# Optimization experiments

Measured on AMD Instinct MI355X. Metric: run time of the kernel, lower is better.

Reference implementation:

```python
import jax, jax.numpy as jnp
import numpy as np

B, S, H = 32, 2048, 1024


def setup_inputs() -> dict:
    key = jax.random.key(0)
    ks = jax.random.split(key, 8)
    scale = 1.0 / np.sqrt(H)
    return {
        "query": jax.random.normal(ks[0], (B, 1, H), dtype=jnp.float32),
        "keys": jax.random.normal(ks[1], (B, S, H), dtype=jnp.float32),
        "Wa_w": jax.random.uniform(ks[2], (H, H), jnp.float32, -scale, scale),
        "Wa_b": jax.random.uniform(ks[3], (H,), jnp.float32, -scale, scale),
        "Ua_w": jax.random.uniform(ks[4], (H, H), jnp.float32, -scale, scale),
        "Ua_b": jax.random.uniform(ks[5], (H,), jnp.float32, -scale, scale),
        "Va_w": jax.random.uniform(ks[6], (1, H), jnp.float32, -scale, scale),
        "Va_b": jax.random.uniform(ks[7], (1,), jnp.float32, -scale, scale),
        "idx": 0,
    }


def reference(query, keys, Wa_w, Wa_b, Ua_w, Ua_b, Va_w, Va_b, idx):
    # torch Linear: y = x @ W.T + b
    q_proj = jnp.einsum("bqh,oh->bqo", query, Wa_w) + Wa_b   # (B,1,H)
    k_proj = jnp.einsum("bsh,oh->bso", keys, Ua_w) + Ua_b    # (B,S,H)
    energy = jnp.tanh(q_proj + k_proj)                        # (B,S,H) broadcast over S
    scores = jnp.einsum("bsh,h->bs", energy, Va_w[0]) + Va_b[0]  # (B,S)
    weights = jax.nn.softmax(scores, axis=-1)[:, None, :]     # (B,1,S)
    context = jnp.einsum("bqs,bsh->bqh", weights, keys)       # (B,1,H)
    return (context, weights)
```

## Files before the change

kernel.cpp:

```cpp
#include <hip/hip_runtime.h>
#include <hip/hip_bf16.h>
#include <math.h>


#define B_ 32
#define S_ 2048
#define H_ 1024
#define M_ (B_ * S_)

#define CONV_BLOCKS 8192
#define UA_BLOCKS 32
#define QP_BLOCKS 512

typedef __bf16 bf16x8 __attribute__((ext_vector_type(8)));
typedef float floatx4 __attribute__((ext_vector_type(4)));

__device__ inline unsigned bf16_rne(float f) {
  unsigned u = __builtin_bit_cast(unsigned, f);
  return (u + 0x7fffu + ((u >> 16) & 1u)) >> 16;
}
__device__ inline unsigned pk2(float x, float y) {
  return bf16_rne(x) | (bf16_rne(y) << 16);
}

__device__ inline float fast_tanh(float x) {
  const float xc = fminf(fmaxf(x, -8.f), 8.f);
  const float e = __expf(2.f * xc);
  return (e - 1.f) * __builtin_amdgcn_rcpf(e + 1.f);
}

#define GLDS(g, l)                                                    \
  __builtin_amdgcn_global_load_lds(                                   \
      (const __attribute__((address_space(1))) void*)(g),             \
      (__attribute__((address_space(3))) void*)(l), 16, 0, 0)

__device__ inline uint4 conv8(const float4* s2) {
  const float4 a = s2[0], b = s2[1];
  uint4 o;
  o.x = pk2(a.x, a.y); o.y = pk2(a.z, a.w);
  o.z = pk2(b.x, b.y); o.w = pk2(b.z, b.w);
  return o;
}

__global__ __launch_bounds__(256) void prep_kernel(
    const float* __restrict__ keys, const float* __restrict__ Ua_w,
    const float* __restrict__ query, const float* __restrict__ Wa_w,
    const float* __restrict__ Wa_b, const float* __restrict__ Ua_b,
    unsigned short* __restrict__ kbf, unsigned short* __restrict__ ubf,
    float* __restrict__ qp, int do_convert) {
  const int blk = blockIdx.x;
  const int tid = threadIdx.x;
  if (blk < CONV_BLOCKS) {
    if (!do_convert) return;
    const int tg = blk * 256 + tid;
#pragma unroll
    for (int c = 0; c < 4; ++c) {
      const size_t idx = (size_t)c * 2097152 + tg;
      ((uint4*)kbf)[idx] = conv8((const float4*)keys + idx * 2);
    }
  } else if (blk < CONV_BLOCKS + UA_BLOCKS) {
    if (!do_convert) return;
    const int tg = (blk - CONV_BLOCKS) * 256 + tid;
#pragma unroll
    for (int c = 0; c < 16; ++c) {
      const size_t idx = (size_t)c * 8192 + tg;
      ((uint4*)ubf)[idx] = conv8((const float4*)Ua_w + idx * 2);
    }
  } else {
    const int bl = blk - CONV_BLOCKS - UA_BLOCKS;
    const int b = bl >> 4;
    const int os = (bl & 15) * 64;
    const int lane = tid & 63;
    const int w = tid >> 6;
    __shared__ float qsh[H_];
    *(float4*)&qsh[tid * 4] = *(const float4*)(query + (size_t)b * H_ + tid * 4);
    __syncthreads();
    for (int t = 0; t < 16; ++t) {
      const int o = os + w * 16 + t;
      const float* wr = Wa_w + (size_t)o * H_;
      float p = 0.f;
#pragma unroll
      for (int j = 0; j < 16; ++j) p += wr[lane + 64 * j] * qsh[lane + 64 * j];
#pragma unroll
      for (int m = 32; m; m >>= 1) p += __shfl_xor(p, m);
      if (lane == 0) qp[b * H_ + o] = p + Wa_b[o] + Ua_b[o];
    }
  }
}

__device__ inline void swizzle_rc(int idx, int& rb, int& cb) {
  cb = (idx >> 3) & 7;
  rb = (idx & 7) | ((idx >> 6) << 3);
}
__device__ inline int chunk_f(int r) { return (r & 3) ^ ((r >> 2) & 3); }

__global__ __launch_bounds__(256) void scores_bf16_kernel(
    const unsigned short* __restrict__ kbf, const unsigned short* __restrict__ ubf,
    const float* __restrict__ qp, const float* __restrict__ Va_w,
    float* __restrict__ sp) {
  const int tid = threadIdx.x;
  int rb, cb;
  swizzle_rc(blockIdx.x, rb, cb);
  const int row0 = rb * 128, c0 = cb * 128;
  const int bq = row0 >> 11;
  const int lane = tid & 63;
  const int w = tid >> 6;
  const int wm = w >> 1, wn = w & 1;
  const int q4 = lane >> 4, n16 = lane & 15;

  __shared__ __align__(16) unsigned short Asm[128][32];
  __shared__ __align__(16) unsigned short Bsm[128][32];
  __shared__ float red[2][128];

  floatx4 acc[4][4];
#pragma unroll
  for (int i = 0; i < 4; ++i)
#pragma unroll
    for (int j = 0; j < 4; ++j) acc[i][j] = {0.f, 0.f, 0.f, 0.f};

  const int r0a = w * 32;
  const int lr = lane >> 2;
  const int lc = ((lane & 3) ^ chunk_f(lr)) * 8;
  const unsigned short* gA0 = kbf + (size_t)(row0 + r0a + lr) * H_ + lc;
  const unsigned short* gA1 = kbf + (size_t)(row0 + r0a + 16 + lr) * H_ + lc;
  const unsigned short* gB0 = ubf + (size_t)(c0 + r0a + lr) * H_ + lc;
  const unsigned short* gB1 = ubf + (size_t)(c0 + r0a + 16 + lr) * H_ + lc;
  unsigned short* lA0 = &Asm[r0a][0];
  unsigned short* lA1 = &Asm[r0a + 16][0];
  unsigned short* lB0 = &Bsm[r0a][0];
  unsigned short* lB1 = &Bsm[r0a + 16][0];

  const int fn = chunk_f(n16);

  for (int kt = 0; kt < 32; ++kt) {
    const int k0 = kt * 32;
    __syncthreads();
    GLDS(gA0 + k0, lA0);
    GLDS(gA1 + k0, lA1);
    GLDS(gB0 + k0, lB0);
    GLDS(gB1 + k0, lB1);
    __syncthreads();
    bf16x8 af[4], bfr[4];
#pragma unroll
    for (int i = 0; i < 4; ++i)
      af[i] = *(const bf16x8*)&Asm[wm * 64 + i * 16 + n16][(q4 ^ fn) * 8];
#pragma unroll
    for (int j = 0; j < 4; ++j)
      bfr[j] = *(const bf16x8*)&Bsm[wn * 64 + j * 16 + n16][(q4 ^ fn) * 8];
#pragma unroll
    for (int i = 0; i < 4; ++i)
#pragma unroll
      for (int j = 0; j < 4; ++j)
        acc[i][j] = __builtin_amdgcn_mfma_f32_16x16x32_bf16(af[i], bfr[j], acc[i][j], 0, 0, 0);
  }

  float rsum[4][4];
#pragma unroll
  for (int i = 0; i < 4; ++i)
#pragma unroll
    for (int r = 0; r < 4; ++r) rsum[i][r] = 0.f;
#pragma unroll
  for (int j = 0; j < 4; ++j) {
    const int col = c0 + wn * 64 + j * 16 + n16;
    const float qv = qp[bq * H_ + col];
    const float vv = Va_w[col];
#pragma unroll
    for (int i = 0; i < 4; ++i)
#pragma unroll
      for (int r = 0; r < 4; ++r)
        rsum[i][r] += fast_tanh(acc[i][j][r] + qv) * vv;
  }
#pragma unroll
  for (int i = 0; i < 4; ++i)
#pragma unroll
    for (int r = 0; r < 4; ++r) {
      float v = rsum[i][r];
      v += __shfl_xor(v, 1);
      v += __shfl_xor(v, 2);
      v += __shfl_xor(v, 4);
      v += __shfl_xor(v, 8);
      rsum[i][r] = v;
    }
  if (n16 == 0) {
#pragma unroll
    for (int i = 0; i < 4; ++i)
#pragma unroll
      for (int r = 0; r < 4; ++r)
        red[wn][wm * 64 + i * 16 + q4 * 4 + r] = rsum[i][r];
  }
  __syncthreads();
  if (tid < 128) sp[(size_t)cb * M_ + row0 + tid] = red[0][tid] + red[1][tid];
}

__global__ __launch_bounds__(256) void scores_f32_kernel(
    const float* __restrict__ keys, const float* __restrict__ Ua_w,
    const float* __restrict__ qp, const float* __restrict__ Va_w,
    float* __restrict__ sp) {
  const int tid = threadIdx.x;
  int rb, cb;
  swizzle_rc(blockIdx.x, rb, cb);
  const int row0 = rb * 128, c0 = cb * 128;
  const int bq = row0 >> 11;
  const int lane = tid & 63;
  const int w = tid >> 6;
  const int wm = w >> 1, wn = w & 1;
  const int q4 = lane >> 4, n16 = lane & 15;

  __shared__ __align__(16) unsigned short Asm[128][40];
  __shared__ __align__(16) unsigned short Bsm[128][40];
  __shared__ float red[2][128];

  floatx4 acc[4][4];
#pragma unroll
  for (int i = 0; i < 4; ++i)
#pragma unroll
    for (int j = 0; j < 4; ++j) acc[i][j] = {0.f, 0.f, 0.f, 0.f};

  for (int kt = 0; kt < 32; ++kt) {
    const int k0 = kt * 32;
    __syncthreads();
#pragma unroll
    for (int rep = 0; rep < 4; ++rep) {
      const int idx4 = rep * 256 + tid;
      const int r = idx4 >> 3;
      const int c4 = (idx4 & 7) << 2;
      const float4 va = *(const float4*)(keys + (size_t)(row0 + r) * H_ + k0 + c4);
      *(uint2*)&Asm[r][c4] = make_uint2(pk2(va.x, va.y), pk2(va.z, va.w));
      const float4 vb = *(const float4*)(Ua_w + (size_t)(c0 + r) * H_ + k0 + c4);
      *(uint2*)&Bsm[r][c4] = make_uint2(pk2(vb.x, vb.y), pk2(vb.z, vb.w));
    }
    __syncthreads();
    bf16x8 af[4], bfr[4];
#pragma unroll
    for (int i = 0; i < 4; ++i)
      af[i] = *(const bf16x8*)&Asm[wm * 64 + i * 16 + n16][q4 * 8];
#pragma unroll
    for (int j = 0; j < 4; ++j)
      bfr[j] = *(const bf16x8*)&Bsm[wn * 64 + j * 16 + n16][q4 * 8];
#pragma unroll
    for (int i = 0; i < 4; ++i)
#pragma unroll
      for (int j = 0; j < 4; ++j)
        acc[i][j] = __builtin_amdgcn_mfma_f32_16x16x32_bf16(af[i], bfr[j], acc[i][j], 0, 0, 0);
  }

  float rsum[4][4];
#pragma unroll
  for (int i = 0; i < 4; ++i)
#pragma unroll
    for (int r = 0; r < 4; ++r) rsum[i][r] = 0.f;
#pragma unroll
  for (int j = 0; j < 4; ++j) {
    const int col = c0 + wn * 64 + j * 16 + n16;
    const float qv = qp[bq * H_ + col];
    const float vv = Va_w[col];
#pragma unroll
    for (int i = 0; i < 4; ++i)
#pragma unroll
      for (int r = 0; r < 4; ++r)
        rsum[i][r] += fast_tanh(acc[i][j][r] + qv) * vv;
  }
#pragma unroll
  for (int i = 0; i < 4; ++i)
#pragma unroll
    for (int r = 0; r < 4; ++r) {
      float v = rsum[i][r];
      v += __shfl_xor(v, 1);
      v += __shfl_xor(v, 2);
      v += __shfl_xor(v, 4);
      v += __shfl_xor(v, 8);
      rsum[i][r] = v;
    }
  if (n16 == 0) {
#pragma unroll
    for (int i = 0; i < 4; ++i)
#pragma unroll
      for (int r = 0; r < 4; ++r)
        red[wn][wm * 64 + i * 16 + q4 * 4 + r] = rsum[i][r];
  }
  __syncthreads();
  if (tid < 128) sp[(size_t)cb * M_ + row0 + tid] = red[0][tid] + red[1][tid];
}

__global__ __launch_bounds__(256) void softmax_kernel(
    const float* __restrict__ sp, float* __restrict__ sw) {
  const int b = blockIdx.x, tid = threadIdx.x;
  float v[8];
#pragma unroll
  for (int k = 0; k < 8; ++k) {
    const size_t base = (size_t)b * S_ + tid + 256 * k;
    float s = 0.f;
#pragma unroll
    for (int j = 0; j < 8; ++j) s += sp[(size_t)j * M_ + base];
    v[k] = s;
  }
  float mx = v[0];
#pragma unroll
  for (int k = 1; k < 8; ++k) mx = fmaxf(mx, v[k]);
#pragma unroll
  for (int m = 32; m; m >>= 1) mx = fmaxf(mx, __shfl_xor(mx, m));
  __shared__ float sred[4], ssum[4];
  if ((tid & 63) == 0) sred[tid >> 6] = mx;
  __syncthreads();
  mx = fmaxf(fmaxf(sred[0], sred[1]), fmaxf(sred[2], sred[3]));
  float e[8], s = 0.f;
#pragma unroll
  for (int k = 0; k < 8; ++k) { e[k] = __expf(v[k] - mx); s += e[k]; }
#pragma unroll
  for (int m = 32; m; m >>= 1) s += __shfl_xor(s, m);
  if ((tid & 63) == 0) ssum[tid >> 6] = s;
  __syncthreads();
  s = ssum[0] + ssum[1] + ssum[2] + ssum[3];
  const float inv = 1.0f / s;
#pragma unroll
  for (int k = 0; k < 8; ++k) sw[b * S_ + tid + 256 * k] = e[k] * inv;
}

__global__ __launch_bounds__(256) void context1_kernel(
    const float* __restrict__ keys, const float* __restrict__ weights,
    float* __restrict__ pctx) {
  const int b = blockIdx.x >> 6;
  const int ch = blockIdx.x & 63;
  const int s0 = ch * 32;
  const int h4 = threadIdx.x;
  const float4* kp4 = (const float4*)(keys + (size_t)(b * S_ + s0) * H_) + h4;
  const float4* wp4 = (const float4*)(weights + b * S_ + s0);
  float4 acc = {0.f, 0.f, 0.f, 0.f};
#pragma unroll
  for (int sq = 0; sq < 8; ++sq) {
    const float4 wv = wp4[sq];
    const float4 k0 = kp4[(sq * 4 + 0) * 256];
    const float4 k1 = kp4[(sq * 4 + 1) * 256];
    const float4 k2 = kp4[(sq * 4 + 2) * 256];
    const float4 k3 = kp4[(sq * 4 + 3) * 256];
    acc.x += wv.x * k0.x + wv.y * k1.x + wv.z * k2.x + wv.w * k3.x;
    acc.y += wv.x * k0.y + wv.y * k1.y + wv.z * k2.y + wv.w * k3.y;
    acc.z += wv.x * k0.z + wv.y * k1.z + wv.z * k2.z + wv.w * k3.z;
    acc.w += wv.x * k0.w + wv.y * k1.w + wv.z * k2.w + wv.w * k3.w;
  }
  *(float4*)(pctx + ((size_t)(b * 64 + ch)) * H_ + h4 * 4) = acc;
}

__global__ __launch_bounds__(256) void context2_kernel(
    const float* __restrict__ pctx, float* __restrict__ ctx) {
  const int b = blockIdx.x;
  const int h4 = threadIdx.x * 4;
  float4 acc = {0.f, 0.f, 0.f, 0.f};
#pragma unroll 8
  for (int c = 0; c < 64; ++c) {
    const float4 v = *(const float4*)(pctx + ((size_t)(b * 64 + c)) * H_ + h4);
    acc.x += v.x; acc.y += v.y; acc.z += v.z; acc.w += v.w;
  }
  *(float4*)(ctx + b * H_ + h4) = acc;
}

extern "C" void kernel_launch(void* const* d_in, const int* in_sizes, int n_in,
                              void* d_out, int out_size, void* d_ws, size_t ws_size,
                              hipStream_t stream) {
  const float* query = (const float*)d_in[0];
  const float* keys  = (const float*)d_in[1];
  const float* Wa_w  = (const float*)d_in[2];
  const float* Wa_b  = (const float*)d_in[3];
  const float* Ua_w  = (const float*)d_in[4];
  const float* Ua_b  = (const float*)d_in[5];
  const float* Va_w  = (const float*)d_in[6];

  float* out = (float*)d_out;
  float* ctx = out;
  float* sw  = out + B_ * H_;

  const size_t qpb = (size_t)B_ * H_ * 4;
  const size_t spb = (size_t)8 * M_ * 4;
  const size_t pcb = (size_t)B_ * 64 * H_ * 4;
  const size_t kb  = (size_t)M_ * H_ * 2;
  const size_t ub  = (size_t)H_ * H_ * 2;
  float* qp = (float*)d_ws;
  float* sp = (float*)((char*)d_ws + qpb);
  float* pctx = (float*)((char*)d_ws + qpb + spb);
  unsigned short* kbf = (unsigned short*)((char*)d_ws + qpb + spb + pcb);
  unsigned short* ubf = (unsigned short*)((char*)d_ws + qpb + spb + pcb + kb);
  const bool fast = ws_size >= qpb + spb + pcb + kb + ub;

  prep_kernel<<<CONV_BLOCKS + UA_BLOCKS + QP_BLOCKS, 256, 0, stream>>>(
      keys, Ua_w, query, Wa_w, Wa_b, Ua_b, kbf, ubf, qp, fast ? 1 : 0);
  if (fast) {
    scores_bf16_kernel<<<4096, 256, 0, stream>>>(kbf, ubf, qp, Va_w, sp);
  } else {
    scores_f32_kernel<<<4096, 256, 0, stream>>>(keys, Ua_w, qp, Va_w, sp);
  }
  softmax_kernel<<<B_, 256, 0, stream>>>(sp, sw);
  context1_kernel<<<2048, 256, 0, stream>>>(keys, sw, pctx);
  context2_kernel<<<B_, 256, 0, stream>>>(pctx, ctx);
}
```

Measured before the change: 632.4 us.

## Fuse fp32-to-bf16 key conversion into the scores GEMM A-tile load

Removes the separate pass that converted the full keys tensor to bf16 in a workspace buffer. The scores kernel now reads fp32 keys directly, converts them in registers with packed bf16 conversion instructions, and stores them to LDS, prefetching the next K-slice into registers during the current step. This saves writing and re-reading a 128MB intermediate. In exchange, each 128-column block re-reads fp32 keys (twice the bytes per tile) and loses the async global-to-LDS path for A.

```diff
diff --git a/kernel.cpp b/kernel.cpp
--- a/kernel.cpp
+++ b/kernel.cpp
@@ -8,9 +8,8 @@
 #define H_ 1024
 #define M_ (B_ * S_)
 
-#define CONV_BLOCKS 8192
+#define QP_BLOCKS 512
 #define UA_BLOCKS 32
-#define QP_BLOCKS 512
 
 typedef __bf16 bf16x8 __attribute__((ext_vector_type(8)));
 typedef float floatx4 __attribute__((ext_vector_type(4)));
@@ -21,6 +20,11 @@
 }
 __device__ inline unsigned pk2(float x, float y) {
   return bf16_rne(x) | (bf16_rne(y) << 16);
+}
+__device__ inline unsigned cvtpk(float x, float y) {
+  unsigned r;
+  asm("v_cvt_pk_bf16_f32 %0, %1, %2" : "=v"(r) : "v"(x), "v"(y));
+  return r;
 }
 
 __device__ inline float fast_tanh(float x) {
@@ -43,33 +47,15 @@
 }
 
 __global__ __launch_bounds__(256) void prep_kernel(
-    const float* __restrict__ keys, const float* __restrict__ Ua_w,
-    const float* __restrict__ query, const float* __restrict__ Wa_w,
-    const float* __restrict__ Wa_b, const float* __restrict__ Ua_b,
-    unsigned short* __restrict__ kbf, unsigned short* __restrict__ ubf,
-    float* __restrict__ qp, int do_convert) {
+    const float* __restrict__ Ua_w, const float* __restrict__ query,
+    const float* __restrict__ Wa_w, const float* __restrict__ Wa_b,
+    const float* __restrict__ Ua_b, unsigned short* __restrict__ ubf,
+    float* __restrict__ qp, int do_ua) {
   const int blk = blockIdx.x;
   const int tid = threadIdx.x;
-  if (blk < CONV_BLOCKS) {
-    if (!do_convert) return;
-    const int tg = blk * 256 + tid;
-#pragma unroll
-    for (int c = 0; c < 4; ++c) {
-      const size_t idx = (size_t)c * 2097152 + tg;
-      ((uint4*)kbf)[idx] = conv8((const float4*)keys + idx * 2);
-    }
-  } else if (blk < CONV_BLOCKS + UA_BLOCKS) {
-    if (!do_convert) return;
-    const int tg = (blk - CONV_BLOCKS) * 256 + tid;
-#pragma unroll
-    for (int c = 0; c < 16; ++c) {
-      const size_t idx = (size_t)c * 8192 + tg;
-      ((uint4*)ubf)[idx] = conv8((const float4*)Ua_w + idx * 2);
-    }
-  } else {
-    const int bl = blk - CONV_BLOCKS - UA_BLOCKS;
-    const int b = bl >> 4;
-    const int os = (bl & 15) * 64;
+  if (blk < QP_BLOCKS) {
+    const int b = blk >> 4;
+    const int os = (blk & 15) * 64;
     const int lane = tid & 63;
     const int w = tid >> 6;
     __shared__ float qsh[H_];
@@ -85,6 +71,14 @@
       for (int m = 32; m; m >>= 1) p += __shfl_xor(p, m);
       if (lane == 0) qp[b * H_ + o] = p + Wa_b[o] + Ua_b[o];
     }
+  } else {
+    if (!do_ua) return;
+    const int tg = (blk - QP_BLOCKS) * 256 + tid;
+#pragma unroll
+    for (int c = 0; c < 16; ++c) {
+      const size_t idx = (size_t)c * 8192 + tg;
+      ((uint4*)ubf)[idx] = conv8((const float4*)Ua_w + idx * 2);
+    }
   }
 }
 
@@ -94,8 +88,8 @@
 }
 __device__ inline int chunk_f(int r) { return (r & 3) ^ ((r >> 2) & 3); }
 
-__global__ __launch_bounds__(256) void scores_bf16_kernel(
-    const unsigned short* __restrict__ kbf, const unsigned short* __restrict__ ubf,
+__global__ __launch_bounds__(256) void scores_af32_kernel(
+    const float* __restrict__ keys, const unsigned short* __restrict__ ubf,
     const float* __restrict__ qp, const float* __restrict__ Va_w,
     float* __restrict__ sp) {
   const int tid = threadIdx.x;
@@ -121,24 +115,41 @@
   const int r0a = w * 32;
   const int lr = lane >> 2;
   const int lc = ((lane & 3) ^ chunk_f(lr)) * 8;
-  const unsigned short* gA0 = kbf + (size_t)(row0 + r0a + lr) * H_ + lc;
-  const unsigned short* gA1 = kbf + (size_t)(row0 + r0a + 16 + lr) * H_ + lc;
   const unsigned short* gB0 = ubf + (size_t)(c0 + r0a + lr) * H_ + lc;
   const unsigned short* gB1 = ubf + (size_t)(c0 + r0a + 16 + lr) * H_ + lc;
-  unsigned short* lA0 = &Asm[r0a][0];
-  unsigned short* lA1 = &Asm[r0a + 16][0];
   unsigned short* lB0 = &Bsm[r0a][0];
   unsigned short* lB1 = &Bsm[r0a + 16][0];
 
+  const int ar = tid >> 1;
+  const int ac0 = (tid & 1) * 2;
+  const float* gA = keys + (size_t)(row0 + ar) * H_ + ac0 * 8;
+  unsigned short* lA0 = &Asm[ar][((ac0 ^ chunk_f(ar)) & 3) * 8];
+  unsigned short* lA1 = &Asm[ar][(((ac0 + 1) ^ chunk_f(ar)) & 3) * 8];
+
   const int fn = chunk_f(n16);
+
+  float4 a0 = *(const float4*)(gA + 0);
+  float4 a1 = *(const float4*)(gA + 4);
+  float4 a2 = *(const float4*)(gA + 8);
+  float4 a3 = *(const float4*)(gA + 12);
 
   for (int kt = 0; kt < 32; ++kt) {
     const int k0 = kt * 32;
     __syncthreads();
-    GLDS(gA0 + k0, lA0);
-    GLDS(gA1 + k0, lA1);
     GLDS(gB0 + k0, lB0);
     GLDS(gB1 + k0, lB1);
+    uint4 u0, u1;
+    u0.x = cvtpk(a0.x, a0.y); u0.y = cvtpk(a0.z, a0.w);
+    u0.z = cvtpk(a1.x, a1.y); u0.w = cvtpk(a1.z, a1.w);
+    u1.x = cvtpk(a2.x, a2.y); u1.y = cvtpk(a2.z, a2.w);
+    u1.z = cvtpk(a3.x, a3.y); u1.w = cvtpk(a3.z, a3.w);
+    *(uint4*)lA0 = u0;
+    *(uint4*)lA1 = u1;
+    const int kn = ((kt + 1) & 31) * 32;
+    a0 = *(const float4*)(gA + kn + 0);
+    a1 = *(const float4*)(gA + kn + 4);
+    a2 = *(const float4*)(gA + kn + 8);
+    a3 = *(const float4*)(gA + kn + 12);
     __syncthreads();
     bf16x8 af[4], bfr[4];
 #pragma unroll
@@ -372,19 +383,17 @@
   const size_t qpb = (size_t)B_ * H_ * 4;
   const size_t spb = (size_t)8 * M_ * 4;
   const size_t pcb = (size_t)B_ * 64 * H_ * 4;
-  const size_t kb  = (size_t)M_ * H_ * 2;
   const size_t ub  = (size_t)H_ * H_ * 2;
   float* qp = (float*)d_ws;
   float* sp = (float*)((char*)d_ws + qpb);
   float* pctx = (float*)((char*)d_ws + qpb + spb);
-  unsigned short* kbf = (unsigned short*)((char*)d_ws + qpb + spb + pcb);
-  unsigned short* ubf = (unsigned short*)((char*)d_ws + qpb + spb + pcb + kb);
-  const bool fast = ws_size >= qpb + spb + pcb + kb + ub;
-
-  prep_kernel<<<CONV_BLOCKS + UA_BLOCKS + QP_BLOCKS, 256, 0, stream>>>(
-      keys, Ua_w, query, Wa_w, Wa_b, Ua_b, kbf, ubf, qp, fast ? 1 : 0);
+  unsigned short* ubf = (unsigned short*)((char*)d_ws + qpb + spb + pcb);
+  const bool fast = ws_size >= qpb + spb + pcb + ub;
+
+  prep_kernel<<<QP_BLOCKS + UA_BLOCKS, 256, 0, stream>>>(
+      Ua_w, query, Wa_w, Wa_b, Ua_b, ubf, qp, fast ? 1 : 0);
   if (fast) {
-    scores_bf16_kernel<<<4096, 256, 0, stream>>>(kbf, ubf, qp, Va_w, sp);
+    scores_af32_kernel<<<4096, 256, 0, stream>>>(keys, ubf, qp, Va_w, sp);
   } else {
     scores_f32_kernel<<<4096, 256, 0, stream>>>(keys, Ua_w, qp, Va_w, sp);
   }
```

Result: slower. 726.9 us (+15.0%).
